# Optimization experiments

Measured on AMD Instinct MI355X. Metric: run time of the kernel, lower is better.

## Reference

```python
import jax, jax.numpy as jnp
import numpy as np
import math

B, S, SIG, EMB, LAT, H, L_ENC, L_DEC = 16, 1024, 256, 256, 256, 8, 2, 2
EH, DH = EMB // H, LAT // H
EPS = 1e-10


def _sinusoidal_last_row(d):
    # last row of a standard sinusoidal PE table (position index = max_len-1)
    pos = 5000.0 - 1.0
    i = np.arange(d)
    angles = pos / np.power(10000.0, (2 * (i // 2)) / d)
    pe = np.where(i % 2 == 0, np.sin(angles), np.cos(angles))
    return jnp.asarray(pe, dtype=jnp.float32)


def setup_inputs() -> dict:
    key = jax.random.key(0)
    ks = iter(jax.random.split(key, 64))
    w = lambda *sh: 0.05 * jax.random.normal(next(ks), sh, dtype=jnp.float32)
    z = lambda *sh: jnp.zeros(sh, dtype=jnp.float32)
    d = {
        'inputData': jax.random.normal(next(ks), (B, S, SIG), dtype=jnp.float32),
        'pos_enc': _sinusoidal_last_row(SIG),
        'embW': w(SIG, EMB), 'embb': z(EMB),
        'qW': w(EMB, EMB), 'qb': z(EMB),
        'kW': w(EMB, EMB), 'kb': z(EMB),
        'vW': w(EMB, EMB), 'vb': z(EMB),
        'encBW': w(EH, EH), 'encBb': z(EH),
        'oW': w(EMB, EMB), 'ob': z(EMB),
        'ffe_W1': w(EMB, 2 * EMB), 'ffe_b1': z(2 * EMB),
        'ffe_W2': w(2 * EMB, EMB), 'ffe_b2': z(EMB),
        'lnSA_g': jnp.ones((L_ENC, EMB)), 'lnSA_b': z(L_ENC, EMB),
        'lnFF_g': jnp.ones((L_ENC, EMB)), 'lnFF_b': z(L_ENC, EMB),
        'start': w(1, LAT),
        'decQW': w(LAT, LAT), 'decQb': z(LAT),
        'decKW': w(EMB, EMB), 'decKb': z(EMB),
        'decVW': w(EMB, LAT), 'decVb': z(LAT),
        'decBW': w(EH + DH, DH), 'decBb': z(DH),
        'latW': w(LAT, LAT), 'latb': z(LAT),
        'ffd_W1': w(LAT, LAT // 2), 'ffd_b1': z(LAT // 2),
        'ffd_W2': w(LAT // 2, LAT), 'ffd_b2': z(LAT),
        'lnCA_g': jnp.ones((L_DEC, LAT)), 'lnCA_b': z(L_DEC, LAT),
        'lnLFF_g': jnp.ones((L_DEC, LAT)), 'lnLFF_b': z(L_DEC, LAT),
        'finW': w(LAT, LAT), 'finb': z(LAT),
    }
    return d


def _ln(x, g, b):
    m = x.mean(-1, keepdims=True)
    v = x.var(-1, keepdims=True)
    return (x - m) * jax.lax.rsqrt(v + EPS) * g + b


def _enc_attn(x, qW, qb, kW, kb, vW, vb, bW, bb, oW, ob):
    # x: (B,S,EMB) -> heads (B,H,S,EH)
    sp = lambda t: t.reshape(B, S, H, EH).transpose(0, 2, 1, 3)
    q, k, v = sp(x @ qW + qb), sp(x @ kW + kb), sp(x @ vW + vb)
    bk = k @ bW + bb                                   # bilinear key (B,H,S,EH)
    attn = jax.nn.softmax(jnp.einsum('bhqd,bhkd->bhqk', q, bk) / math.sqrt(EH), axis=-1)
    out = jnp.einsum('bhqk,bhkd->bhqd', attn, v)
    out = out.transpose(0, 2, 1, 3).reshape(B, S, EMB)
    return out @ oW + ob


def _dec_attn(enc, lat, qW, qb, kW, kb, vW, vb, bW, bb, oW, ob):
    # lat: (B,LAT) single query token; enc: (B,S,EMB)
    q = (lat @ qW + qb).reshape(B, 1, H, DH).transpose(0, 2, 1, 3)   # (B,H,1,DH)
    k = (enc @ kW + kb).reshape(B, S, H, EH).transpose(0, 2, 1, 3)   # (B,H,S,EH)
    v = (enc @ vW + vb).reshape(B, S, H, DH).transpose(0, 2, 1, 3)   # (B,H,S,DH)
    qcat = jnp.broadcast_to(q, (B, H, S, DH))
    kcat = jnp.concatenate([k, qcat], axis=-1)                       # (B,H,S,EH+DH)
    bk = kcat @ bW + bb                                              # (B,H,S,DH)
    attn = jax.nn.softmax(jnp.einsum('bhqd,bhkd->bhqk', q, bk) / math.sqrt(EH + DH), axis=-1)
    out = jnp.einsum('bhqk,bhkd->bhqd', attn, v)                     # (B,H,1,DH)
    out = out.transpose(0, 2, 1, 3).reshape(B, LAT)
    return out @ oW + ob


def reference(inputData, pos_enc, embW, embb, qW, qb, kW, kb, vW, vb, encBW, encBb,
              oW, ob, ffe_W1, ffe_b1, ffe_W2, ffe_b2, lnSA_g, lnSA_b, lnFF_g, lnFF_b,
              start, decQW, decQb, decKW, decKb, decVW, decVb, decBW, decBb,
              latW, latb, ffd_W1, ffd_b1, ffd_W2, ffd_b2, lnCA_g, lnCA_b,
              lnLFF_g, lnLFF_b, finW, finb):
    emb = (inputData + pos_enc) @ embW + embb          # (B,S,EMB)
    t = emb
    for l in range(L_ENC):
        n = _ln(t, lnSA_g[l], lnSA_b[l])
        a = _enc_attn(n, qW, qb, kW, kb, vW, vb, encBW, encBb, oW, ob) + n
        t = a + emb
        n2 = _ln(t, lnFF_g[l], lnFF_b[l])
        ff = jax.nn.selu(n2 @ ffe_W1 + ffe_b1) @ ffe_W2 + ffe_b2
        t = ff + n2
    init_lat = jnp.broadcast_to(start, (B, LAT))
    lat = init_lat
    for l in range(L_DEC):
        nl = _ln(init_lat, lnCA_g[l], lnCA_b[l])       # module always feeds initialLatentData
        lat = _dec_attn(t, nl, decQW, decQb, decKW, decKb, decVW, decVb,
                        decBW, decBb, latW, latb)
        nf = _ln(lat, lnLFF_g[l], lnLFF_b[l])
        lat = jax.nn.selu(nf @ ffd_W1 + ffd_b1) @ ffd_W2 + ffd_b2
    return lat @ finW + finb
```

## Files before the change

### kernel.cpp

```cpp
#include <hip/hip_runtime.h>
#include <hip/hip_bf16.h>
#include <math.h>

typedef __hip_bfloat16 bf16;

#define BB 16
#define SS 1024
#define NH 8
#define NR (BB*SS)
#define SZE ((size_t)NR*256)
#define RS 264
#define HS 520

typedef __attribute__((ext_vector_type(8))) short short8;
typedef __attribute__((ext_vector_type(4))) float f32x4;
typedef __attribute__((ext_vector_type(8))) unsigned short u16x8;
typedef __attribute__((ext_vector_type(4))) unsigned short u16x4;

__device__ __forceinline__ float bf2f(bf16 x){ return __bfloat162float(x); }
__device__ __forceinline__ bf16  f2bf(float x){ return __float2bfloat16(x); }
__device__ __forceinline__ unsigned short f2bfu(float x){
  bf16 t = __float2bfloat16(x); return *reinterpret_cast<unsigned short*>(&t);
}
__device__ __forceinline__ float bfu2f(unsigned short u){
  return __uint_as_float(((unsigned)u)<<16);
}

__device__ __forceinline__ float ldT(const float* p, size_t i){ return p[i]; }
__device__ __forceinline__ float ldT(const bf16*  p, size_t i){ return bf2f(p[i]); }
__device__ __forceinline__ void  stT(float* p, size_t i, float v){ p[i] = v; }
__device__ __forceinline__ void  stT(bf16*  p, size_t i, float v){ p[i] = f2bf(v); }

__device__ __forceinline__ float selu_f(float x){
  const float a = 1.6732632423543772f, sc = 1.0507009873554805f;
  return sc * (x > 0.f ? x : a * expm1f(x));
}

__device__ __forceinline__ void gload16(const void* g, void* l){
  __builtin_amdgcn_global_load_lds(
      (const __attribute__((address_space(1))) unsigned int*)g,
      (__attribute__((address_space(3))) unsigned int*)l, 16, 0, 0);
}

struct PtrPack { const void* p[43]; };
struct TabPack { int off[43]; int cnt[43]; int total; };
struct TrTab   { int srcOff[12]; int K[12]; int N[12]; int dstOff[12]; int total; };

__global__ __launch_bounds__(256) void k_canon(PtrPack ptrs, TabPack tab,
    float* __restrict__ dst, int* __restrict__ flagw)
{
  unsigned w0 = ((const unsigned*)ptrs.p[18])[0];
  int isbf = (w0 == 0x3F803F80u) ? 1 : 0;
  if (blockIdx.x == 0 && threadIdx.x == 0) *flagw = isbf;
  __shared__ int so[43], sn[43];
  int tid = threadIdx.x;
  if (tid < 43){ so[tid] = tab.off[tid]; sn[tid] = tab.cnt[tid]; }
  __syncthreads();
  int g = blockIdx.x*256 + tid;
  if (g >= tab.total) return;
  int seg = 1;
  while (seg < 42 && g >= so[seg] + sn[seg]) seg++;
  int li = g - so[seg];
  float v = isbf ? bf2f(((const bf16*)ptrs.p[seg])[li])
                 : ((const float*)ptrs.p[seg])[li];
  dst[g] = v;
}

__global__ __launch_bounds__(256) void k_transW(const float* __restrict__ wt,
    TrTab tt, unsigned short* __restrict__ dst)
{
  int g = blockIdx.x*256 + threadIdx.x;
  if (g >= tt.total) return;
  int seg = 0;
  while (seg < 11 && g >= tt.dstOff[seg] + tt.K[seg]*tt.N[seg]) seg++;
  int li = g - tt.dstOff[seg];
  int K = tt.K[seg], N = tt.N[seg];
  int n = li / K, k = li - n*K;
  dst[g] = f2bfu(wt[tt.srcOff[seg] + (size_t)k*N + n]);
}

__global__ __launch_bounds__(256) void k_qfold(const float* __restrict__ wt,
    int qOff, int qbOff, int bwOff, unsigned short* __restrict__ qW2t,
    float* __restrict__ qbf)
{
  __shared__ float bw[32];
  int n = blockIdx.x, t = threadIdx.x;
  int h = n>>5, d = n&31;
  if (t < 32) bw[t] = wt[bwOff + d*32 + t];
  __syncthreads();
  float acc = 0.f;
  #pragma unroll 8
  for (int j = 0; j < 32; j++) acc += wt[qOff + (size_t)t*256 + h*32 + j]*bw[j];
  qW2t[(size_t)n*256 + t] = f2bfu(acc);
  if (t == 0){
    float a = 0.f;
    #pragma unroll 8
    for (int j = 0; j < 32; j++) a += wt[qbOff + h*32 + j]*bw[j];
    qbf[n] = a;
  }
}

template<int K, int LDA, int CT>
__device__ __forceinline__ void wave_gemmN(const unsigned short (*As)[LDA],
    const unsigned short* __restrict__ Wt, int n0, f32x4 acc[4][CT], int lane)
{
  int col = lane & 15, quad = lane >> 4;
  #pragma unroll
  for (int k0 = 0; k0 < K; k0 += 32){
    short8 a[4], b[CT];
    #pragma unroll
    for (int rt = 0; rt < 4; rt++)
      a[rt] = *(const short8*)(&As[rt*16 + col][k0 + quad*8]);
    #pragma unroll
    for (int ct = 0; ct < CT; ct++)
      b[ct] = *(const short8*)(&Wt[(size_t)(n0 + ct*16 + col)*K + k0 + quad*8]);
    #pragma unroll
    for (int rt = 0; rt < 4; rt++)
      #pragma unroll
      for (int ct = 0; ct < CT; ct++)
        acc[rt][ct] = __builtin_amdgcn_mfma_f32_16x16x32_bf16(a[rt], b[ct], acc[rt][ct], 0, 0, 0);
  }
}

template<int K, int LDA, int CT>
__device__ __forceinline__ void wave_gemmM32(const unsigned short (*As)[LDA],
    const unsigned short* __restrict__ Wt, int n0, f32x4 acc[2][CT], int lane)
{
  int col = lane & 15, quad = lane >> 4;
  #pragma unroll
  for (int k0 = 0; k0 < K; k0 += 32){
    short8 a[2], b[CT];
    #pragma unroll
    for (int rt = 0; rt < 2; rt++)
      a[rt] = *(const short8*)(&As[rt*16 + col][k0 + quad*8]);
    #pragma unroll
    for (int ct = 0; ct < CT; ct++)
      b[ct] = *(const short8*)(&Wt[(size_t)(n0 + ct*16 + col)*K + k0 + quad*8]);
    #pragma unroll
    for (int rt = 0; rt < 2; rt++)
      #pragma unroll
      for (int ct = 0; ct < CT; ct++)
        acc[rt][ct] = __builtin_amdgcn_mfma_f32_16x16x32_bf16(a[rt], b[ct], acc[rt][ct], 0, 0, 0);
  }
}

#define ZERO_ACC4(acc)  { _Pragma("unroll") for (int rt=0;rt<4;rt++){ _Pragma("unroll") for (int ct=0;ct<4;ct++) acc[rt][ct] = (f32x4){0.f,0.f,0.f,0.f}; } }
#define ZERO_ACC2(acc)  { _Pragma("unroll") for (int rt=0;rt<4;rt++){ _Pragma("unroll") for (int ct=0;ct<2;ct++) acc[rt][ct] = (f32x4){0.f,0.f,0.f,0.f}; } }
#define ZERO_ACC24(acc) { _Pragma("unroll") for (int rt=0;rt<2;rt++){ _Pragma("unroll") for (int ct=0;ct<4;ct++) acc[rt][ct] = (f32x4){0.f,0.f,0.f,0.f}; } }

#define EPI_BEGIN(e) { int rt = (e)>>4, ct = ((e)>>2)&3, r = (e)&3; \
    int lrow = rt*16 + quad*4 + r; int gcol0 = ct*16 + col; \
    float av = acc[rt][ct][r]; (void)lrow; (void)gcol0; (void)av;
#define EPI_END }

#define EPI32_BEGIN(e) { int rt = (e)>>4, ct = ((e)>>2)&3, r = (e)&3; \
    int lrow = rt*16 + quad*4 + r; int gcol0 = ct*16 + col; \
    float av = acc[rt][ct][r]; (void)lrow; (void)gcol0; (void)av;
#define EPI32_END }

template<int PRE, typename OT>
__global__ __launch_bounds__(256) void k_gemm_mfma(const void* __restrict__ A,
    const int* __restrict__ flagp, const float* __restrict__ pe,
    const unsigned short* __restrict__ Wt, const float* __restrict__ bias,
    OT* __restrict__ out)
{
  __shared__ __align__(16) unsigned short As[64][RS];
  int tid = threadIdx.x;
  int m = blockIdx.x & 255, nh = blockIdx.x >> 8;
  int row0 = m*64;
  if (PRE == 0){
    int f = *flagp;
    for (int jj = 0; jj < 64; jj++){
      int idx = tid + jj*256, row = idx>>8, c = idx&255;
      size_t g = (size_t)(row0+row)*256 + c;
      float x = f ? bf2f(((const bf16*)A)[g]) : ((const float*)A)[g];
      As[row][c] = f2bfu(x + pe[c]);
    }
  } else {
    for (int jj = 0; jj < 16; jj++){
      int idx = tid + jj*256;
      int row = idx>>6, c4 = (idx&63)<<2;
      float4 x = *(const float4*)((const float*)A + (size_t)(row0+row)*256 + c4);
      *(u16x4*)(&As[row][c4]) = (u16x4){f2bfu(x.x),f2bfu(x.y),f2bfu(x.z),f2bfu(x.w)};
    }
  }
  __syncthreads();
  int w = tid>>6, lane = tid&63, col = lane&15, quad = lane>>4;
  int n0 = nh*128 + w*32;
  f32x4 acc[4][2];
  ZERO_ACC2(acc);
  wave_gemmN<256, RS, 2>(As, Wt, n0, acc, lane);
  #pragma unroll
  for (int rt = 0; rt < 4; rt++){
    #pragma unroll
    for (int ct = 0; ct < 2; ct++){
      #pragma unroll
      for (int r = 0; r < 4; r++){
        int grow = row0 + rt*16 + quad*4 + r;
        int gcol = n0 + ct*16 + col;
        stT(out, (size_t)grow*256 + gcol, acc[rt][ct][r] + bias[gcol]);
      }
    }
  }
}

__global__ __launch_bounds__(256) void k_decKV(const float* __restrict__ A,
    const unsigned short* __restrict__ KWt, const float* __restrict__ kb,
    const unsigned short* __restrict__ VWt, const float* __restrict__ vb,
    bf16* __restrict__ ko, bf16* __restrict__ vo)
{
  __shared__ __align__(16) unsigned short As[64][RS];
  int tid = threadIdx.x;
  int m = blockIdx.x & 255, nh = blockIdx.x >> 8;
  int row0 = m*64;
  for (int jj = 0; jj < 16; jj++){
    int idx = tid + jj*256;
    int row = idx>>6, c4 = (idx&63)<<2;
    float4 x = *(const float4*)(A + (size_t)(row0+row)*256 + c4);
    *(u16x4*)(&As[row][c4]) = (u16x4){f2bfu(x.x),f2bfu(x.y),f2bfu(x.z),f2bfu(x.w)};
  }
  __syncthreads();
  int w = tid>>6, lane = tid&63, col = lane&15, quad = lane>>4;
  int n0 = nh*128 + w*32;
  f32x4 acc[4][2];
  ZERO_ACC2(acc);
  wave_gemmN<256, RS, 2>(As, KWt, n0, acc, lane);
  #pragma unroll
  for (int rt = 0; rt < 4; rt++){
    #pragma unroll
    for (int ct = 0; ct < 2; ct++){
      #pragma unroll
      for (int r = 0; r < 4; r++){
        int grow = row0 + rt*16 + quad*4 + r;
        int gcol = n0 + ct*16 + col;
        ko[(size_t)grow*256 + gcol] = f2bf(acc[rt][ct][r] + kb[gcol]);
      }
    }
  }
  ZERO_ACC2(acc);
  wave_gemmN<256, RS, 2>(As, VWt, n0, acc, lane);
  #pragma unroll
  for (int rt = 0; rt < 4; rt++){
    #pragma unroll
    for (int ct = 0; ct < 2; ct++){
      #pragma unroll
      for (int r = 0; r < 4; r++){
        int grow = row0 + rt*16 + quad*4 + r;
        int gcol = n0 + ct*16 + col;
        vo[(size_t)grow*256 + gcol] = f2bf(acc[rt][ct][r] + vb[gcol]);
      }
    }
  }
}

__global__ __launch_bounds__(256) void k_qkvbk_mfma(const float* __restrict__ tsrc,
    const float* __restrict__ lng, const float* __restrict__ lnb,
    const unsigned short* __restrict__ qW2t, const float* __restrict__ qbf,
    const unsigned short* __restrict__ kWt, const float* __restrict__ kb,
    const unsigned short* __restrict__ vWt, const float* __restrict__ vb,
    bf16* __restrict__ qo, bf16* __restrict__ vo, bf16* __restrict__ bko)
{
  __shared__ __align__(16) unsigned short Ns[64][RS];
  __shared__ float mArr[64], rArr[64];
  int tid = threadIdx.x;
  int m = blockIdx.x & 255, nh = blockIdx.x >> 8;
  int row0 = m*64;
  int b = row0 >> 10, s0 = row0 & 1023;
  {
    int row = tid>>2, l4 = tid&3;
    const float4* rp = (const float4*)(tsrc + (size_t)(row0+row)*256) + l4*16;
    float s = 0.f, s2 = 0.f;
    #pragma unroll 4
    for (int c = 0; c < 16; c++){
      float4 x = rp[c];
      s += x.x + x.y + x.z + x.w;
      s2 += x.x*x.x + x.y*x.y + x.z*x.z + x.w*x.w;
    }
    s  += __shfl_down(s, 2, 4);  s  += __shfl_down(s, 1, 4);
    s2 += __shfl_down(s2, 2, 4); s2 += __shfl_down(s2, 1, 4);
    if (l4 == 0){
      float mn = s*(1.f/256.f);
      float v = s2*(1.f/256.f) - mn*mn;
      mArr[row] = mn; rArr[row] = rsqrtf(fmaxf(v,0.f) + 1e-10f);
    }
  }
  __syncthreads();
  for (int jj = 0; jj < 16; jj++){
    int idx = tid + jj*256;
    int row = idx>>6, c4 = (idx&63)<<2;
    float4 x = *(const float4*)(tsrc + (size_t)(row0+row)*256 + c4);
    float mn = mArr[row], rr = rArr[row];
    u16x4 o;
    o[0] = f2bfu((x.x - mn)*rr*lng[c4+0] + lnb[c4+0]);
    o[1] = f2bfu((x.y - mn)*rr*lng[c4+1] + lnb[c4+1]);
    o[2] = f2bfu((x.z - mn)*rr*lng[c4+2] + lnb[c4+2]);
    o[3] = f2bfu((x.w - mn)*rr*lng[c4+3] + lnb[c4+3]);
    *(u16x4*)(&Ns[row][c4]) = o;
  }
  __syncthreads();
  int w = tid>>6, lane = tid&63, col = lane&15, quad = lane>>4;
  int n0 = nh*128 + w*32;
  f32x4 acc[4][2];
  ZERO_ACC2(acc);
  wave_gemmN<256, RS, 2>(Ns, qW2t, n0, acc, lane);
  #pragma unroll
  for (int rt = 0; rt < 4; rt++){
    #pragma unroll
    for (int ct = 0; ct < 2; ct++){
      #pragma unroll
      for (int r = 0; r < 4; r++){
        int grow = row0 + rt*16 + quad*4 + r;
        int gcol = n0 + ct*16 + col;
        qo[(size_t)grow*256 + gcol] = f2bf(acc[rt][ct][r] + qbf[gcol]);
      }
    }
  }
  ZERO_ACC2(acc);
  wave_gemmN<256, RS, 2>(Ns, vWt, n0, acc, lane);
  #pragma unroll
  for (int rt = 0; rt < 4; rt++){
    #pragma unroll
    for (int ct = 0; ct < 2; ct++){
      #pragma unroll
      for (int r = 0; r < 4; r++){
        int grow = row0 + rt*16 + quad*4 + r;
        int gcol = n0 + ct*16 + col;
        vo[(size_t)grow*256 + gcol] = f2bf(acc[rt][ct][r] + vb[gcol]);
      }
    }
  }
  ZERO_ACC2(acc);
  wave_gemmN<256, RS, 2>(Ns, kWt, n0, acc, lane);
  int h = nh*4 + w;
  #pragma unroll
  for (int rt = 0; rt < 4; rt++){
    #pragma unroll
    for (int ct = 0; ct < 2; ct++){
      #pragma unroll
      for (int r = 0; r < 4; r++){
        int srow = s0 + rt*16 + quad*4 + r;
        int d = ct*16 + col;
        bko[(((size_t)(b*NH+h))*SS + srow)*32 + d] =
            f2bf(acc[rt][ct][r] + kb[h*32 + d]);
      }
    }
  }
}

__global__ __launch_bounds__(256) void k_attn_mfma(
    const bf16* __restrict__ q, const bf16* __restrict__ bk,
    const bf16* __restrict__ v, bf16* __restrict__ ao)
{
  int bi = blockIdx.x;
  int qq = bi >> 7, b = (bi >> 3) & 15, h = bi & 7;
  int tid = threadIdx.x;
  int w = tid>>6, lane = tid&63;
  int quad = lane>>4, col = lane&15;
  int q0 = qq*128 + w*32;

  __shared__ __align__(16) unsigned short Ks2b[2][64][32];
  __shared__ __align__(16) unsigned short Vt2b[2][32][76];

  const float scale2 = 0.17677669529663687f * 1.4426950408889634f;
  short8 aq[2];
  #pragma unroll
  for (int rt = 0; rt < 2; rt++){
    const unsigned short* gq = (const unsigned short*)q
        + ((size_t)(b*SS + q0 + rt*16 + col))*256 + h*32 + quad*8;
    u16x8 qv = *(const u16x8*)gq;
    #pragma unroll
    for (int i=0;i<8;i++) aq[rt][i] = (short)f2bfu(bfu2f(qv[i])*scale2);
  }

  float l_r[2] = {0.f, 0.f};
  f32x4 o[2][2];
  #pragma unroll
  for (int rt=0;rt<2;rt++)
    #pragma unroll
    for (int ct=0;ct<2;ct++) o[rt][ct] = (f32x4){0.f,0.f,0.f,0.f};

  int krow = tid>>2, ksl = tid&3;
  int kslw = ksl ^ ((krow>>1)&3);
  int vk0 = tid>>3, vdg = tid&7;
  int vk1 = vk0 + 32;
  int rsl = (quad ^ ((col>>1)&3))*8;

  const unsigned short* bkp = (const unsigned short*)bk + ((size_t)(b*NH+h))*SS*32;
  const unsigned short* vp  = (const unsigned short*)v + (size_t)b*SS*256 + h*32;

  u16x8 rK;
  u16x4 rV0, rV1;
  rK  = *(const u16x8*)(bkp + (size_t)krow*32 + ksl*8);
  rV0 = *(const u16x4*)(vp + (size_t)vk0*256 + vdg*4);
  rV1 = *(const u16x4*)(vp + (size_t)vk1*256 + vdg*4);

  for (int kt = 0; kt < 16; kt++){
    int cb = kt & 1;
    *(u16x8*)(&Ks2b[cb][krow][kslw*8]) = rK;
    #pragma unroll
    for (int i=0;i<4;i++) Vt2b[cb][vdg*4+i][vk0] = rV0[i];
    #pragma unroll
    for (int i=0;i<4;i++) Vt2b[cb][vdg*4+i][vk1] = rV1[i];
    __syncthreads();
    if (kt < 15){
      int nk = kt + 1;
      rK  = *(const u16x8*)(bkp + (size_t)(nk*64 + krow)*32 + ksl*8);
      rV0 = *(const u16x4*)(vp + (size_t)(nk*64 + vk0)*256 + vdg*4);
      rV1 = *(const u16x4*)(vp + (size_t)(nk*64 + vk1)*256 + vdg*4);
    }
    #pragma unroll
    for (int g = 0; g < 2; g++){
      unsigned pk[2][4];
      #pragma unroll
      for (int tt = 0; tt < 2; tt++){
        int t4 = g*2 + tt;
        short8 bk8 = *(const short8*)(&Ks2b[cb][t4*16 + col][rsl]);
        #pragma unroll
        for (int rt = 0; rt < 2; rt++){
          f32x4 s = __builtin_amdgcn_mfma_f32_16x16x32_bf16(bk8, aq[rt],
                      (f32x4){0.f,0.f,0.f,0.f}, 0, 0, 0);
          float e0 = __builtin_amdgcn_exp2f(s[0]);
          float e1 = __builtin_amdgcn_exp2f(s[1]);
          float e2 = __builtin_amdgcn_exp2f(s[2]);
          float e3 = __builtin_amdgcn_exp2f(s[3]);
          l_r[rt] += (e0+e1)+(e2+e3);
          pk[rt][tt*2+0] = __builtin_amdgcn_perm(
              __float_as_uint(e1), __float_as_uint(e0), 0x07060302u);
          pk[rt][tt*2+1] = __builtin_amdgcn_perm(
// ... 25 lines not shown
  for (int rt=0;rt<2;rt++){
    float l = l_r[rt];
    l += __shfl_xor(l, 16, 64);
    l += __shfl_xor(l, 32, 64);
    float inv = 1.f / l;
    size_t obase = ((size_t)(b*SS + q0 + rt*16 + col))*256 + h*32;
    #pragma unroll
    for (int ct=0;ct<2;ct++){
      u16x4 ov;
      #pragma unroll
      for (int r=0;r<4;r++) ov[r] = f2bfu(o[rt][ct][r]*inv);
      *(u16x4*)((unsigned short*)ao + obase + ct*16 + quad*4) = ov;
    }
  }
}

__global__ __launch_bounds__(256) void k_oln_mfma(
    const float* __restrict__ tsrc, const float* __restrict__ emb,
    const bf16* __restrict__ ao,
    const float* __restrict__ lnSAg, const float* __restrict__ lnSAb,
    const unsigned short* __restrict__ oWt, const float* __restrict__ ob,
    const float* __restrict__ lnFFg, const float* __restrict__ lnFFb,
    bf16* __restrict__ n2o)
{
  __shared__ __align__(16) unsigned short Aos[32][RS];
  __shared__ __align__(16) unsigned short Tm[32][RS];
  __shared__ float mArr[32], rArr[32];
  int tid = threadIdx.x, row0 = blockIdx.x*32;
  {
    int row = tid>>3, l8 = tid&7;
    const float* rp = tsrc + (size_t)(row0+row)*256;
    float s = 0.f, s2 = 0.f;
    for (int c = l8; c < 256; c += 8){ float x = rp[c]; s += x; s2 += x*x; }
    s  += __shfl_down(s, 4, 8);  s  += __shfl_down(s, 2, 8);  s  += __shfl_down(s, 1, 8);
    s2 += __shfl_down(s2, 4, 8); s2 += __shfl_down(s2, 2, 8); s2 += __shfl_down(s2, 1, 8);
    if (l8 == 0){
      float m = s*(1.f/256.f);
      float v = s2*(1.f/256.f) - m*m;
      mArr[row] = m; rArr[row] = rsqrtf(fmaxf(v,0.f) + 1e-10f);
    }
  }
  for (int jj = 0; jj < 4; jj++){
    int idx = tid + jj*256;
    int row = idx>>5, c8 = idx&31;
    *(u16x8*)(&Aos[row][c8*8]) =
        *(const u16x8*)((const unsigned short*)ao + (size_t)(row0+row)*256 + c8*8);
  }
  __syncthreads();
  int w = tid>>6, lane = tid&63, col = lane&15, quad = lane>>4;
  f32x4 acc[2][4];
  ZERO_ACC24(acc);
  wave_gemmM32<256, RS, 4>(Aos, oWt, w*64, acc, lane);
  #pragma unroll
  for (int e = 0; e < 32; e++){
    EPI32_BEGIN(e)
    int gcol = w*64 + gcol0;
    size_t g = (size_t)(row0+lrow)*256 + gcol;
    float n1 = (tsrc[g] - mArr[lrow])*rArr[lrow]*lnSAg[gcol] + lnSAb[gcol];
    Tm[lrow][gcol] = f2bfu(av + ob[gcol] + n1 + emb[g]);
    EPI32_END
  }
  __syncthreads();
  {
    int row = tid>>3, l8 = tid&7;
    float s = 0.f, s2 = 0.f;
    for (int c = l8; c < 256; c += 8){ float x = bfu2f(Tm[row][c]); s += x; s2 += x*x; }
    s  += __shfl_down(s, 4, 8);  s  += __shfl_down(s, 2, 8);  s  += __shfl_down(s, 1, 8);
    s2 += __shfl_down(s2, 4, 8); s2 += __shfl_down(s2, 2, 8); s2 += __shfl_down(s2, 1, 8);
    if (l8 == 0){
      float m = s*(1.f/256.f);
      float v = s2*(1.f/256.f) - m*m;
      mArr[row] = m; rArr[row] = rsqrtf(fmaxf(v,0.f) + 1e-10f);
    }
  }
  __syncthreads();
  for (int jj = 0; jj < 32; jj++){
    int idx = tid + jj*256, row = idx>>8, c = idx&255;
    float x = bfu2f(Tm[row][c]);
    n2o[(size_t)(row0+row)*256 + c] =
        f2bf((x - mArr[row])*rArr[row]*lnFFg[c] + lnFFb[c]);
  }
}

#define FF_STAGE(B, KT) { \
  int k0 = (KT)*64; \
  _Pragma("unroll") \
  for (int i = 0; i < 4; i++){ int c = w*4 + i; \
    gload16(A  + (size_t)(row0 + c*8 + rsub)*KFULL + k0 + sgo, &As[B][c*512]); } \
  _Pragma("unroll") \
  for (int i = 0; i < 2; i++){ int c = w*2 + i; \
    gload16(Wb + (size_t)(n0   + c*8 + rsub)*KFULL + k0 + sgo, &Bs[B][c*512]); } }

#define FF_COMPUTE(B) { \
  _Pragma("unroll") \
  for (int kk = 0; kk < 2; kk++){ \
    short8 a[4], b2r[2]; \
    _Pragma("unroll") \
    for (int rt = 0; rt < 4; rt++) \
      a[rt] = *(const short8*)(&As[B][((wr*64 + rt*16 + col)<<6) + ((((kk<<2)|quad) ^ (col&7))<<3)]); \
    _Pragma("unroll") \
    for (int ct = 0; ct < 2; ct++) \
      b2r[ct] = *(const short8*)(&Bs[B][((wc*32 + ct*16 + col)<<6) + ((((kk<<2)|quad) ^ (col&7))<<3)]); \
    _Pragma("unroll") \
    for (int rt = 0; rt < 4; rt++) \
      _Pragma("unroll") \
      for (int ct = 0; ct < 2; ct++) \
        acc[rt][ct] = __builtin_amdgcn_mfma_f32_16x16x32_bf16(a[rt], b2r[ct], acc[rt][ct], 0, 0, 0); } }

template<int KFULL, int NFULL, int EPI>
__global__ __launch_bounds__(256) void k_ff_gemm(const bf16* __restrict__ A,
    const unsigned short* __restrict__ Wt, const float* __restrict__ bias,
    const bf16* __restrict__ res, void* __restrict__ outv)
{
  __shared__ __align__(16) unsigned short As[2][128*64];
  __shared__ __align__(16) unsigned short Bs[2][64*64];
  constexpr int NWG = 128 * (NFULL/64);
  constexpr int NKT = KFULL/64;
  int tid = threadIdx.x;
  int w = tid>>6, lane = tid&63;
  int col = lane&15, quad = lane>>4;
  int wr = w>>1, wc = w&1;
  int rsub = lane>>3;
  int sgo = (((lane&7) ^ rsub)<<3);
  int bid = blockIdx.x;
  int swz = (bid & 7)*(NWG>>3) + (bid >> 3);
  int mb = swz & 127, nb = swz >> 7;
  int row0 = mb*128, n0 = nb*64;
  const bf16* Wb = (const bf16*)Wt;

  f32x4 acc[4][2];
  ZERO_ACC2(acc);

  FF_STAGE(0, 0);
  __syncthreads();
  #pragma unroll
  for (int kt = 0; kt < NKT-1; kt++){
    int cb = kt & 1;
    FF_STAGE(cb^1, kt+1);
    FF_COMPUTE(cb);
    __syncthreads();
  }
  FF_COMPUTE((NKT-1)&1);

  if (EPI == 0){
    bf16* o = (bf16*)outv;
    #pragma unroll
    for (int rt = 0; rt < 4; rt++){
      #pragma unroll
      for (int ct = 0; ct < 2; ct++){
        #pragma unroll
        for (int r = 0; r < 4; r++){
          int grow = row0 + wr*64 + rt*16 + quad*4 + r;
          int gcol = n0 + wc*32 + ct*16 + col;
          o[(size_t)grow*NFULL + gcol] = f2bf(selu_f(acc[rt][ct][r] + bias[gcol]));
        }
      }
    }
  } else {
    float* o = (float*)outv;
    #pragma unroll
    for (int rt = 0; rt < 4; rt++){
      #pragma unroll
      for (int ct = 0; ct < 2; ct++){
        #pragma unroll
        for (int r = 0; r < 4; r++){
          int grow = row0 + wr*64 + rt*16 + quad*4 + r;
          int gcol = n0 + wc*32 + ct*16 + col;
          size_t g = (size_t)grow*NFULL + gcol;
          o[g] = acc[rt][ct][r] + bias[gcol] + bf2f(res[g]);
        }
      }
    }
  }
}

__global__ __launch_bounds__(256) void k_dec_head(const float* __restrict__ startp,
    const float* __restrict__ lng, const float* __restrict__ lnb,
    const float* __restrict__ decQW, const float* __restrict__ decQb,
    const float* __restrict__ decBW,
    float* __restrict__ s_q, float* __restrict__ s_qc)
{
  __shared__ float s1[256], s2[256], nl[256], qv[256];
  int t = threadIdx.x;
  float v = startp[t];
  s1[t]=v; s2[t]=v*v; __syncthreads();
  for (int s=128;s>0;s>>=1){
    if (t<s){ s1[t]+=s1[t+s]; s2[t]+=s2[t+s]; }
    __syncthreads();
  }
  float m = s1[0]*(1.f/256.f);
  float var = s2[0]*(1.f/256.f) - m*m;
  float r = rsqrtf(fmaxf(var,0.f) + 1e-10f);
  nl[t] = (v-m)*r*lng[t] + lnb[t];
  __syncthreads();
  float acc = decQb[t];
  for (int k=0;k<256;k++) acc += nl[k]*decQW[k*256+t];
  qv[t] = acc; s_q[t] = acc;
  __syncthreads();
  int h = t>>5, d = t&31;
  float a = 0.f;
  #pragma unroll 8
  for (int e=0;e<32;e++) a += qv[h*32+e]*decBW[(32+e)*32 + d];
  s_qc[t] = a;
}

__global__ __launch_bounds__(256) void k_bkdec_mfma(const bf16* __restrict__ kk,
    const float* __restrict__ qc, const unsigned short* __restrict__ decBWt,
    const float* __restrict__ Bb, bf16* __restrict__ bko)
{
  __shared__ __align__(16) unsigned short Ks[64][RS];
  int tid = threadIdx.x, row0 = blockIdx.x*64;
  int b = row0 >> 10, s0 = row0 & 1023;
  for (int jj = 0; jj < 8; jj++){
    int idx = tid + jj*256;
    int row = idx>>5, c8 = idx&31;
    *(u16x8*)(&Ks[row][c8*8]) =
        *(const u16x8*)((const unsigned short*)kk + (size_t)(row0+row)*256 + c8*8);
  }
  __syncthreads();
  int w = tid>>6, lane = tid&63, col = lane&15, quad = lane>>4;
  f32x4 acc[4][4];
  ZERO_ACC4(acc);
  #pragma unroll
  for (int ct = 0; ct < 4; ct++){
    int base = w*64 + ct*16;
    int h = base >> 5, d0 = base & 31;
    short8 bfrag = *(const short8*)(&decBWt[(size_t)(d0 + col)*32 + quad*8]);
    #pragma unroll
    for (int rt = 0; rt < 4; rt++){
      short8 afrag = *(const short8*)(&Ks[rt*16 + col][h*32 + quad*8]);
      acc[rt][ct] = __builtin_amdgcn_mfma_f32_16x16x32_bf16(afrag, bfrag, acc[rt][ct], 0, 0, 0);
    }
  }
  #pragma unroll
  for (int e = 0; e < 64; e++){
    EPI_BEGIN(e)
    int srow = s0 + lrow;
    int gcol = w*64 + gcol0;
    int h = gcol >> 5, d = gcol & 31;
    bko[(((size_t)(b*NH+h))*SS + srow)*32 + d] = f2bf(av + qc[gcol] + Bb[d]);
    EPI_END
  }
}

__global__ __launch_bounds__(256) void k_attn_dec(const float* __restrict__ q,
    const bf16* __restrict__ bk, const bf16* __restrict__ v,
    float* __restrict__ out)
{
  int h = blockIdx.x & 7, b = blockIdx.x >> 3;
  int tid = threadIdx.x;
  __shared__ float qs[32];
  __shared__ float sc[SS];
  __shared__ float red[256];
  if (tid < 32) qs[tid] = q[h*32 + tid] * (0.125f * 1.4426950408889634f);
  __syncthreads();
  float lsum = 0.f;
  for (int jj=0;jj<4;jj++){
    int j = tid*4 + jj;
// ... 14 lines not shown
    acc += sc[j]*bf2f(v[((size_t)(b*SS + j))*256 + h*32 + d]);
  red[c*32+d] = acc;
  __syncthreads();
  if (tid < 32){
    float s = 0.f;
    #pragma unroll
    for (int cc=0;cc<8;cc++) s += red[cc*32+tid];
    out[b*256 + h*32 + tid] = s / gs;
  }
}

__global__ __launch_bounds__(256) void k_dec_tail(const float* __restrict__ s_ao,
    const float* __restrict__ latW, const float* __restrict__ latb,
    const float* __restrict__ lng, const float* __restrict__ lnb,
    const float* __restrict__ W1, const float* __restrict__ b1,
    const float* __restrict__ W2, const float* __restrict__ b2,
    const float* __restrict__ finW, const float* __restrict__ finb,
    const int* __restrict__ flagp, void* __restrict__ outv)
{
  __shared__ float x[256], y[256], s1[256], s2[256];
  int t = threadIdx.x, b = blockIdx.x;
  x[t] = s_ao[b*256 + t];
  __syncthreads();
  float lat = latb[t];
  for (int k=0;k<256;k++) lat += x[k]*latW[k*256+t];
  s1[t]=lat; s2[t]=lat*lat; __syncthreads();
  for (int s=128;s>0;s>>=1){
    if (t<s){ s1[t]+=s1[t+s]; s2[t]+=s2[t+s]; }
    __syncthreads();
  }
  float m = s1[0]*(1.f/256.f);
  float var = s2[0]*(1.f/256.f) - m*m;
  float r = rsqrtf(fmaxf(var,0.f) + 1e-10f);
  y[t] = (lat-m)*r*lng[t] + lnb[t];
  __syncthreads();
  if (t < 128){
    float a2 = b1[t];
    for (int k=0;k<256;k++) a2 += y[k]*W1[k*128+t];
    x[t] = selu_f(a2);
  }
  __syncthreads();
  float a3 = b2[t];
  for (int k=0;k<128;k++) a3 += x[k]*W2[k*256+t];
  s1[t] = a3;
  __syncthreads();
  float o = finb[t];
  for (int k=0;k<256;k++) o += s1[k]*finW[k*256+t];
  size_t oi = (size_t)b*256 + t;
  if (*flagp) ((bf16*)outv)[oi] = f2bf(o);
  else        ((float*)outv)[oi] = o;
}

extern "C" void kernel_launch(void* const* d_in, const int* in_sizes, int n_in,
                              void* d_out, int out_size, void* d_ws, size_t ws_size,
                              hipStream_t stream)
{
  static const int cnts[43] = {
    0,256,65536,256,65536,256,65536,256,65536,256,1024,32,65536,256,
    131072,512,131072,256,512,512,512,512,256,65536,256,65536,256,65536,256,
    2048,32,65536,256,32768,128,32768,256,512,512,512,512,65536,256 };
  TabPack tab; int acc0 = 0;
  for (int i = 0; i < 43; i++){ tab.off[i] = acc0; tab.cnt[i] = cnts[i]; acc0 += cnts[i]; }
  tab.total = acc0;
  PtrPack ptrs;
  for (int i = 0; i < 43; i++) ptrs.p[i] = d_in[i];

  char* p = (char*)d_ws;
  float* wt   = (float*)p;
  int*  flagp = (int*)(p + (4u<<20));
  char* bigc  = p + (4u<<20) + 256;
  float* g_emb = (float*)bigc;
  float* g_t   = (float*)(bigc + SZE*4);
  bf16*  g_q   = (bf16*)(bigc + 2*SZE*4);
  bf16*  g_v   = (bf16*)(bigc + 2*SZE*4 + SZE*2);
  bf16*  g_ao  = (bf16*)(bigc + 2*SZE*4 + 2*SZE*2);
  bf16*  g_bk  = (bf16*)(bigc + 2*SZE*4 + 3*SZE*2);
  float* fsm   = (float*)(bigc + 2*SZE*4 + 4*SZE*2);
  unsigned short* wtr = (unsigned short*)(bigc + 2*SZE*4 + 4*SZE*2 + 131072*4);
  float* s_q  = fsm;
  float* s_qc = fsm + 256;
  float* s_ao = fsm + 512;
  float* qbf  = fsm + 8192;
  bf16*  g_h1 = g_v;

  static const int trIdx[10] = {2,4,6,8,12,14,16,25,27,10};
  static const int trK[10]   = {256,256,256,256,256,256,512,256,256,32};
  static const int trN[10]   = {256,256,256,256,256,512,256,256,256,32};
  TrTab tr; int tacc = 0;
  for (int i = 0; i < 10; i++){
    tr.srcOff[i] = tab.off[trIdx[i]];
    tr.K[i] = trK[i]; tr.N[i] = trN[i];
    tr.dstOff[i] = tacc; tacc += trK[i]*trN[i];
  }
  tr.srcOff[10] = tab.off[29];        tr.K[10]=32; tr.N[10]=32; tr.dstOff[10]=tacc; tacc+=1024;
  tr.srcOff[11] = tab.off[29] + 1024; tr.K[11]=32; tr.N[11]=32; tr.dstOff[11]=tacc; tacc+=1024;
  tr.total = tacc;
  const unsigned short *embWt = wtr + tr.dstOff[0],
    *kWt = wtr + tr.dstOff[2], *vWt = wtr + tr.dstOff[3], *oWt = wtr + tr.dstOff[4],
    *ffeW1t = wtr + tr.dstOff[5], *ffeW2t = wtr + tr.dstOff[6],
    *decKWt = wtr + tr.dstOff[7], *decVWt = wtr + tr.dstOff[8],
    *decBWtk = wtr + tr.dstOff[10];
  unsigned short* qW2t = wtr + tr.total;

  #define WP(i) (wt + tab.off[i])
  const float *pe=WP(1), *embb=WP(3), *qb=WP(5), *kb=WP(7), *vb=WP(9),
    *ob=WP(13), *ffeb1=WP(15), *ffeb2=WP(17),
    *lnSAg=WP(18), *lnSAb=WP(19), *lnFFg=WP(20), *lnFFb=WP(21),
    *startp=WP(22), *decQW=WP(23), *decQb=WP(24), *decKb=WP(26),
    *decVb=WP(28), *decBW=WP(29), *decBb=WP(30), *latW=WP(31),
    *latb=WP(32), *ffdW1=WP(33), *ffdb1=WP(34), *ffdW2=WP(35), *ffdb2=WP(36),
    *lnCAg=WP(37), *lnCAb=WP(38), *lnLFFg=WP(39), *lnLFFb=WP(40),
    *finW=WP(41), *finb=WP(42);

  dim3 blk(256);
  const int G64  = NR/64;
  const int G32  = NR/32;
  const int GSP  = 512;
  const int GA2  = 1024;
  const int LD   = 1;

  k_canon<<<(tab.total+255)/256, blk, 0, stream>>>(ptrs, tab, wt, flagp);
  k_transW<<<(tr.total+255)/256, blk, 0, stream>>>(wt, tr, wtr);
  k_qfold<<<256, blk, 0, stream>>>(wt, tab.off[4], tab.off[5], tab.off[10], qW2t, qbf);

  k_gemm_mfma<0,float><<<GSP, blk, 0, stream>>>(d_in[0], flagp, pe, embWt, embb, g_emb);

  const float* tcur = g_emb;
  for (int l = 0; l < 2; l++){
    k_qkvbk_mfma<<<GSP, blk, 0, stream>>>(tcur, lnSAg+l*256, lnSAb+l*256,
        qW2t, qbf, kWt, kb, vWt, vb, g_q, g_v, g_bk);
    k_attn_mfma<<<GA2, blk, 0, stream>>>(g_q, g_bk, g_v, g_ao);
    k_oln_mfma<<<G32, blk, 0, stream>>>(tcur, g_emb, g_ao,
        lnSAg+l*256, lnSAb+l*256, oWt, ob, lnFFg+l*256, lnFFb+l*256, g_q);
    k_ff_gemm<256,512,0><<<1024, blk, 0, stream>>>(g_q, ffeW1t, ffeb1, (const bf16*)nullptr, g_h1);
    k_ff_gemm<512,256,1><<<512, blk, 0, stream>>>(g_h1, ffeW2t, ffeb2, g_q, g_t);
    tcur = g_t;
  }

  k_dec_head<<<1, blk, 0, stream>>>(startp, lnCAg+LD*256, lnCAb+LD*256,
      decQW, decQb, decBW, s_q, s_qc);
  k_decKV<<<GSP, blk, 0, stream>>>(g_t, decKWt, decKb, decVWt, decVb, g_q, g_v);
  k_bkdec_mfma<<<G64, blk, 0, stream>>>(g_q, s_qc, decBWtk, decBb, g_bk);
  k_attn_dec<<<BB*NH, blk, 0, stream>>>(s_q, g_bk, g_v, s_ao);
  k_dec_tail<<<BB, blk, 0, stream>>>(s_ao, latW, latb, lnLFFg+LD*256, lnLFFb+LD*256,
      ffdW1, ffdb1, ffdW2, ffdb2, finW, finb, flagp, d_out);
  #undef WP
}
```

Measured before the change: 501.0 us.

## Split LN from QKV projection and reuse pipelined FF GEMM for QKV and decoder KV

The fused LayerNorm+QKV kernel is split into a standalone LayerNorm kernel that writes bf16, followed by a concatenated QKV GEMM built on the double-buffered global_load_lds FF GEMM machinery with 128x64 tiles. The decoder K/V projection likewise moves to this pipelined GEMM. It now reads a bf16 copy of the final encoder output, which the last FF2 epilogue writes. The aim is to replace the older kernels, which staged all of K=256 in LDS with no pipelining, with the faster tiled GEMM path. The cost is an extra bf16 round trip through global memory for the normalized activations and an extra bf16 store in the last FF2 kernel. The weight-transpose table is reorganized so K, V and folded Q weights sit contiguously, and the transpose kernel's segment search bound is lowered to match.

```diff
diff --git a/kernel.cpp b/kernel.cpp
--- a/kernel.cpp
+++ b/kernel.cpp
@@ -10,7 +10,6 @@
 #define NR (BB*SS)
 #define SZE ((size_t)NR*256)
 #define RS 264
-#define HS 520
 
 typedef __attribute__((ext_vector_type(8))) short short8;
 typedef __attribute__((ext_vector_type(4))) float f32x4;
@@ -26,10 +25,8 @@
   return __uint_as_float(((unsigned)u)<<16);
 }
 
-__device__ __forceinline__ float ldT(const float* p, size_t i){ return p[i]; }
-__device__ __forceinline__ float ldT(const bf16*  p, size_t i){ return bf2f(p[i]); }
-__device__ __forceinline__ void  stT(float* p, size_t i, float v){ p[i] = v; }
-__device__ __forceinline__ void  stT(bf16*  p, size_t i, float v){ p[i] = f2bf(v); }
+__device__ __forceinline__ void stT(float* p, size_t i, float v){ p[i] = v; }
+__device__ __forceinline__ void stT(bf16*  p, size_t i, float v){ p[i] = f2bf(v); }
 
 __device__ __forceinline__ float selu_f(float x){
   const float a = 1.6732632423543772f, sc = 1.0507009873554805f;
@@ -72,7 +69,7 @@
   int g = blockIdx.x*256 + threadIdx.x;
   if (g >= tt.total) return;
   int seg = 0;
-  while (seg < 11 && g >= tt.dstOff[seg] + tt.K[seg]*tt.N[seg]) seg++;
+  while (seg < 8 && g >= tt.dstOff[seg] + tt.K[seg]*tt.N[seg]) seg++;
   int li = g - tt.dstOff[seg];
   int K = tt.K[seg], N = tt.N[seg];
   int n = li / K, k = li - n*K;
@@ -204,68 +201,12 @@
   }
 }
 
-__global__ __launch_bounds__(256) void k_decKV(const float* __restrict__ A,
-    const unsigned short* __restrict__ KWt, const float* __restrict__ kb,
-    const unsigned short* __restrict__ VWt, const float* __restrict__ vb,
-    bf16* __restrict__ ko, bf16* __restrict__ vo)
-{
-  __shared__ __align__(16) unsigned short As[64][RS];
-  int tid = threadIdx.x;
-  int m = blockIdx.x & 255, nh = blockIdx.x >> 8;
-  int row0 = m*64;
-  for (int jj = 0; jj < 16; jj++){
-    int idx = tid + jj*256;
-    int row = idx>>6, c4 = (idx&63)<<2;
-    float4 x = *(const float4*)(A + (size_t)(row0+row)*256 + c4);
-    *(u16x4*)(&As[row][c4]) = (u16x4){f2bfu(x.x),f2bfu(x.y),f2bfu(x.z),f2bfu(x.w)};
-  }
-  __syncthreads();
-  int w = tid>>6, lane = tid&63, col = lane&15, quad = lane>>4;
-  int n0 = nh*128 + w*32;
-  f32x4 acc[4][2];
-  ZERO_ACC2(acc);
-  wave_gemmN<256, RS, 2>(As, KWt, n0, acc, lane);
-  #pragma unroll
-  for (int rt = 0; rt < 4; rt++){
-    #pragma unroll
-    for (int ct = 0; ct < 2; ct++){
-      #pragma unroll
-      for (int r = 0; r < 4; r++){
-        int grow = row0 + rt*16 + quad*4 + r;
-        int gcol = n0 + ct*16 + col;
-        ko[(size_t)grow*256 + gcol] = f2bf(acc[rt][ct][r] + kb[gcol]);
-      }
-    }
-  }
-  ZERO_ACC2(acc);
-  wave_gemmN<256, RS, 2>(As, VWt, n0, acc, lane);
-  #pragma unroll
-  for (int rt = 0; rt < 4; rt++){
-    #pragma unroll
-    for (int ct = 0; ct < 2; ct++){
-      #pragma unroll
-      for (int r = 0; r < 4; r++){
-        int grow = row0 + rt*16 + quad*4 + r;
-        int gcol = n0 + ct*16 + col;
-        vo[(size_t)grow*256 + gcol] = f2bf(acc[rt][ct][r] + vb[gcol]);
-      }
-    }
-  }
-}
-
-__global__ __launch_bounds__(256) void k_qkvbk_mfma(const float* __restrict__ tsrc,
+__global__ __launch_bounds__(256) void k_ln(const float* __restrict__ tsrc,
     const float* __restrict__ lng, const float* __restrict__ lnb,
-    const unsigned short* __restrict__ qW2t, const float* __restrict__ qbf,
-    const unsigned short* __restrict__ kWt, const float* __restrict__ kb,
-    const unsigned short* __restrict__ vWt, const float* __restrict__ vb,
-    bf16* __restrict__ qo, bf16* __restrict__ vo, bf16* __restrict__ bko)
-{
-  __shared__ __align__(16) unsigned short Ns[64][RS];
+    bf16* __restrict__ out)
+{
   __shared__ float mArr[64], rArr[64];
-  int tid = threadIdx.x;
-  int m = blockIdx.x & 255, nh = blockIdx.x >> 8;
-  int row0 = m*64;
-  int b = row0 >> 10, s0 = row0 & 1023;
+  int tid = threadIdx.x, row0 = blockIdx.x*64;
   {
     int row = tid>>2, l4 = tid&3;
     const float4* rp = (const float4*)(tsrc + (size_t)(row0+row)*256) + l4*16;
@@ -295,55 +236,161 @@
     o[1] = f2bfu((x.y - mn)*rr*lng[c4+1] + lnb[c4+1]);
     o[2] = f2bfu((x.z - mn)*rr*lng[c4+2] + lnb[c4+2]);
     o[3] = f2bfu((x.w - mn)*rr*lng[c4+3] + lnb[c4+3]);
-    *(u16x4*)(&Ns[row][c4]) = o;
-  }
-  __syncthreads();
-  int w = tid>>6, lane = tid&63, col = lane&15, quad = lane>>4;
-  int n0 = nh*128 + w*32;
-  f32x4 acc[4][2];
-  ZERO_ACC2(acc);
-  wave_gemmN<256, RS, 2>(Ns, qW2t, n0, acc, lane);
-  #pragma unroll
-  for (int rt = 0; rt < 4; rt++){
-    #pragma unroll
-    for (int ct = 0; ct < 2; ct++){
-      #pragma unroll
-      for (int r = 0; r < 4; r++){
-        int grow = row0 + rt*16 + quad*4 + r;
-        int gcol = n0 + ct*16 + col;
-        qo[(size_t)grow*256 + gcol] = f2bf(acc[rt][ct][r] + qbf[gcol]);
-      }
-    }
-  }
-  ZERO_ACC2(acc);
-  wave_gemmN<256, RS, 2>(Ns, vWt, n0, acc, lane);
-  #pragma unroll
-  for (int rt = 0; rt < 4; rt++){
-    #pragma unroll
-    for (int ct = 0; ct < 2; ct++){
-      #pragma unroll
-      for (int r = 0; r < 4; r++){
-        int grow = row0 + rt*16 + quad*4 + r;
-        int gcol = n0 + ct*16 + col;
-        vo[(size_t)grow*256 + gcol] = f2bf(acc[rt][ct][r] + vb[gcol]);
-      }
-    }
-  }
-  ZERO_ACC2(acc);
-  wave_gemmN<256, RS, 2>(Ns, kWt, n0, acc, lane);
-  int h = nh*4 + w;
-  #pragma unroll
-  for (int rt = 0; rt < 4; rt++){
-    #pragma unroll
-    for (int ct = 0; ct < 2; ct++){
-      #pragma unroll
-      for (int r = 0; r < 4; r++){
-        int srow = s0 + rt*16 + quad*4 + r;
-        int d = ct*16 + col;
-        bko[(((size_t)(b*NH+h))*SS + srow)*32 + d] =
-            f2bf(acc[rt][ct][r] + kb[h*32 + d]);
-      }
-    }
+    *(u16x4*)((unsigned short*)out + (size_t)(row0+row)*256 + c4) = o;
+  }
+}
+
+#define FF_STAGE(B, KT) { \
+  int k0 = (KT)*64; \
+  _Pragma("unroll") \
+  for (int i = 0; i < 4; i++){ int c = w*4 + i; \
+    gload16(A  + (size_t)(row0 + c*8 + rsub)*KFULL + k0 + sgo, &As[B][c*512]); } \
+  _Pragma("unroll") \
+  for (int i = 0; i < 2; i++){ int c = w*2 + i; \
+    gload16(Wb + (size_t)(n0   + c*8 + rsub)*KFULL + k0 + sgo, &Bs[B][c*512]); } }
+
+#define FF_COMPUTE(B) { \
+  _Pragma("unroll") \
+  for (int kk = 0; kk < 2; kk++){ \
+    short8 a[4], b2r[2]; \
+    _Pragma("unroll") \
+    for (int rt = 0; rt < 4; rt++) \
+      a[rt] = *(const short8*)(&As[B][((wr*64 + rt*16 + col)<<6) + ((((kk<<2)|quad) ^ (col&7))<<3)]); \
+    _Pragma("unroll") \
+    for (int ct = 0; ct < 2; ct++) \
+      b2r[ct] = *(const short8*)(&Bs[B][((wc*32 + ct*16 + col)<<6) + ((((kk<<2)|quad) ^ (col&7))<<3)]); \
+    _Pragma("unroll") \
+    for (int rt = 0; rt < 4; rt++) \
+      _Pragma("unroll") \
+      for (int ct = 0; ct < 2; ct++) \
+        acc[rt][ct] = __builtin_amdgcn_mfma_f32_16x16x32_bf16(a[rt], b2r[ct], acc[rt][ct], 0, 0, 0); } }
+
+#define FF_PROLOG() \
+  __shared__ __align__(16) unsigned short As[2][128*64]; \
+  __shared__ __align__(16) unsigned short Bs[2][64*64]; \
+  int tid = threadIdx.x; \
+  int w = tid>>6, lane = tid&63; \
+  int col = lane&15, quad = lane>>4; \
+  int wr = w>>1, wc = w&1; \
+  int rsub = lane>>3; \
+  int sgo = (((lane&7) ^ rsub)<<3); \
+  int bid = blockIdx.x; \
+  int swz = (bid & 7)*(NWG>>3) + (bid >> 3); \
+  int mb = swz & 127, nb = swz >> 7; \
+  int row0 = mb*128, n0 = nb*64; \
+  f32x4 acc[4][2]; \
+  ZERO_ACC2(acc); \
+  FF_STAGE(0, 0); \
+  __syncthreads(); \
+  _Pragma("unroll") \
+  for (int kt = 0; kt < NKT-1; kt++){ \
+    int cb = kt & 1; \
+    FF_STAGE(cb^1, kt+1); \
+    FF_COMPUTE(cb); \
+    __syncthreads(); \
+  } \
+  FF_COMPUTE((NKT-1)&1);
+
+#define FF_EPI_LOOP(body) \
+  _Pragma("unroll") \
+  for (int rt = 0; rt < 4; rt++){ \
+    _Pragma("unroll") \
+    for (int ct = 0; ct < 2; ct++){ \
+      _Pragma("unroll") \
+      for (int r = 0; r < 4; r++){ \
+        int grow = row0 + wr*64 + rt*16 + quad*4 + r; \
+        int lcol = wc*32 + ct*16 + col; \
+        float av = acc[rt][ct][r]; \
+        body \
+      } } }
+
+template<int KFULL, int NFULL, int EPI>
+__global__ __launch_bounds__(256) void k_ff_gemm(const bf16* __restrict__ A,
+    const unsigned short* __restrict__ Wt, const float* __restrict__ bias,
+    const bf16* __restrict__ res, void* __restrict__ outv, bf16* __restrict__ outb)
+{
+  constexpr int NWG = 128 * (NFULL/64);
+  constexpr int NKT = KFULL/64;
+  const bf16* Wb = (const bf16*)Wt;
+  FF_PROLOG()
+  if (EPI == 0){
+    bf16* o = (bf16*)outv;
+    FF_EPI_LOOP({
+      int gcol = n0 + lcol;
+      o[(size_t)grow*NFULL + gcol] = f2bf(selu_f(av + bias[gcol]));
+    })
+  } else if (EPI == 1){
+    float* o = (float*)outv;
+    FF_EPI_LOOP({
+      int gcol = n0 + lcol;
+      size_t g = (size_t)grow*NFULL + gcol;
+      o[g] = av + bias[gcol] + bf2f(res[g]);
+    })
+  } else {
+    float* o = (float*)outv;
+    FF_EPI_LOOP({
+      int gcol = n0 + lcol;
+      size_t g = (size_t)grow*NFULL + gcol;
+      float val = av + bias[gcol] + bf2f(res[g]);
+      o[g] = val;
+      outb[g] = f2bf(val);
+    })
+  }
+}
+
+__global__ __launch_bounds__(256) void k_qkv_gemm(const bf16* __restrict__ A,
+    const unsigned short* __restrict__ Wt,
+    const float* __restrict__ vb, const float* __restrict__ kb,
+    const float* __restrict__ qbf,
+    bf16* __restrict__ qo, bf16* __restrict__ vo, bf16* __restrict__ bko)
+{
+  constexpr int KFULL = 256;
+  constexpr int NWG = 128 * 12;
+  constexpr int NKT = 4;
+  const bf16* Wb = (const bf16*)Wt;
+  FF_PROLOG()
+  if (n0 < 256){
+    FF_EPI_LOOP({
+      int gcol = n0 + lcol;
+      vo[(size_t)grow*256 + gcol] = f2bf(av + vb[gcol]);
+    })
+  } else if (n0 < 512){
+    FF_EPI_LOOP({
+      int kcol = n0 - 256 + lcol;
+      int h = kcol>>5;
+      int d = kcol&31;
+      int b = grow>>10;
+      int srow = grow&1023;
+      bko[(((size_t)(b*NH+h))*SS + srow)*32 + d] = f2bf(av + kb[kcol]);
+    })
+  } else {
+    FF_EPI_LOOP({
+      int qcol = n0 - 512 + lcol;
+      qo[(size_t)grow*256 + qcol] = f2bf(av + qbf[qcol]);
+    })
+  }
+}
+
+__global__ __launch_bounds__(256) void k_decKV_gemm(const bf16* __restrict__ A,
+    const unsigned short* __restrict__ Wt,
+    const float* __restrict__ kbd, const float* __restrict__ vbd,
+    bf16* __restrict__ ko, bf16* __restrict__ vo)
+{
+  constexpr int KFULL = 256;
+  constexpr int NWG = 128 * 8;
+  constexpr int NKT = 4;
+  const bf16* Wb = (const bf16*)Wt;
+  FF_PROLOG()
+  if (n0 < 256){
+    FF_EPI_LOOP({
+      int gcol = n0 + lcol;
+      ko[(size_t)grow*256 + gcol] = f2bf(av + kbd[gcol]);
+    })
+  } else {
+    FF_EPI_LOOP({
+      int gcol = n0 - 256 + lcol;
+      vo[(size_t)grow*256 + gcol] = f2bf(av + vbd[gcol]);
+    })
   }
 }
 
@@ -535,98 +582,6 @@
   }
 }
 
-#define FF_STAGE(B, KT) { \
-  int k0 = (KT)*64; \
-  _Pragma("unroll") \
-  for (int i = 0; i < 4; i++){ int c = w*4 + i; \
-    gload16(A  + (size_t)(row0 + c*8 + rsub)*KFULL + k0 + sgo, &As[B][c*512]); } \
-  _Pragma("unroll") \
-  for (int i = 0; i < 2; i++){ int c = w*2 + i; \
-    gload16(Wb + (size_t)(n0   + c*8 + rsub)*KFULL + k0 + sgo, &Bs[B][c*512]); } }
-
-#define FF_COMPUTE(B) { \
-  _Pragma("unroll") \
-  for (int kk = 0; kk < 2; kk++){ \
-    short8 a[4], b2r[2]; \
-    _Pragma("unroll") \
-    for (int rt = 0; rt < 4; rt++) \
-      a[rt] = *(const short8*)(&As[B][((wr*64 + rt*16 + col)<<6) + ((((kk<<2)|quad) ^ (col&7))<<3)]); \
-    _Pragma("unroll") \
-    for (int ct = 0; ct < 2; ct++) \
-      b2r[ct] = *(const short8*)(&Bs[B][((wc*32 + ct*16 + col)<<6) + ((((kk<<2)|quad) ^ (col&7))<<3)]); \
-    _Pragma("unroll") \
-    for (int rt = 0; rt < 4; rt++) \
-      _Pragma("unroll") \
-      for (int ct = 0; ct < 2; ct++) \
-        acc[rt][ct] = __builtin_amdgcn_mfma_f32_16x16x32_bf16(a[rt], b2r[ct], acc[rt][ct], 0, 0, 0); } }
-
-template<int KFULL, int NFULL, int EPI>
-__global__ __launch_bounds__(256) void k_ff_gemm(const bf16* __restrict__ A,
-    const unsigned short* __restrict__ Wt, const float* __restrict__ bias,
-    const bf16* __restrict__ res, void* __restrict__ outv)
-{
-  __shared__ __align__(16) unsigned short As[2][128*64];
-  __shared__ __align__(16) unsigned short Bs[2][64*64];
-  constexpr int NWG = 128 * (NFULL/64);
-  constexpr int NKT = KFULL/64;
-  int tid = threadIdx.x;
-  int w = tid>>6, lane = tid&63;
-  int col = lane&15, quad = lane>>4;
-  int wr = w>>1, wc = w&1;
-  int rsub = lane>>3;
-  int sgo = (((lane&7) ^ rsub)<<3);
-  int bid = blockIdx.x;
-  int swz = (bid & 7)*(NWG>>3) + (bid >> 3);
-  int mb = swz & 127, nb = swz >> 7;
-  int row0 = mb*128, n0 = nb*64;
-  const bf16* Wb = (const bf16*)Wt;
-
-  f32x4 acc[4][2];
-  ZERO_ACC2(acc);
-
-  FF_STAGE(0, 0);
-  __syncthreads();
-  #pragma unroll
-  for (int kt = 0; kt < NKT-1; kt++){
-    int cb = kt & 1;
-    FF_STAGE(cb^1, kt+1);
-    FF_COMPUTE(cb);
-    __syncthreads();
-  }
-  FF_COMPUTE((NKT-1)&1);
-
-  if (EPI == 0){
-    bf16* o = (bf16*)outv;
-    #pragma unroll
-    for (int rt = 0; rt < 4; rt++){
-      #pragma unroll
-      for (int ct = 0; ct < 2; ct++){
-        #pragma unroll
-        for (int r = 0; r < 4; r++){
-          int grow = row0 + wr*64 + rt*16 + quad*4 + r;
-          int gcol = n0 + wc*32 + ct*16 + col;
-          o[(size_t)grow*NFULL + gcol] = f2bf(selu_f(acc[rt][ct][r] + bias[gcol]));
-        }
-      }
-    }
-  } else {
-    float* o = (float*)outv;
-    #pragma unroll
-    for (int rt = 0; rt < 4; rt++){
-      #pragma unroll
-      for (int ct = 0; ct < 2; ct++){
-        #pragma unroll
-        for (int r = 0; r < 4; r++){
-          int grow = row0 + wr*64 + rt*16 + quad*4 + r;
-          int gcol = n0 + wc*32 + ct*16 + col;
-          size_t g = (size_t)grow*NFULL + gcol;
-          o[g] = acc[rt][ct][r] + bias[gcol] + bf2f(res[g]);
-        }
-      }
-    }
-  }
-}
-
 __global__ __launch_bounds__(256) void k_dec_head(const float* __restrict__ startp,
     const float* __restrict__ lng, const float* __restrict__ lnb,
     const float* __restrict__ decQW, const float* __restrict__ decQb,
@@ -807,28 +762,31 @@
   float* s_ao = fsm + 512;
   float* qbf  = fsm + 8192;
   bf16*  g_h1 = g_v;
-
-  static const int trIdx[10] = {2,4,6,8,12,14,16,25,27,10};
-  static const int trK[10]   = {256,256,256,256,256,256,512,256,256,32};
-  static const int trN[10]   = {256,256,256,256,256,512,256,256,256,32};
+  bf16*  g_n  = g_ao;
+  bf16*  g_tb = g_bk;
+
+  static const int trIdx[6] = {2,12,14,16,25,27};
+  static const int trK[6]   = {256,256,256,512,256,256};
+  static const int trN[6]   = {256,256,512,256,256,256};
   TrTab tr; int tacc = 0;
-  for (int i = 0; i < 10; i++){
+  for (int i = 0; i < 6; i++){
     tr.srcOff[i] = tab.off[trIdx[i]];
     tr.K[i] = trK[i]; tr.N[i] = trN[i];
     tr.dstOff[i] = tacc; tacc += trK[i]*trN[i];
   }
-  tr.srcOff[10] = tab.off[29];        tr.K[10]=32; tr.N[10]=32; tr.dstOff[10]=tacc; tacc+=1024;
-  tr.srcOff[11] = tab.off[29] + 1024; tr.K[11]=32; tr.N[11]=32; tr.dstOff[11]=tacc; tacc+=1024;
+  tr.srcOff[6] = tab.off[29]; tr.K[6]=32;  tr.N[6]=32;  tr.dstOff[6]=tacc; tacc+=1024;
+  tr.srcOff[7] = tab.off[8];  tr.K[7]=256; tr.N[7]=256; tr.dstOff[7]=tacc; tacc+=65536;
+  tr.srcOff[8] = tab.off[6];  tr.K[8]=256; tr.N[8]=256; tr.dstOff[8]=tacc; tacc+=65536;
   tr.total = tacc;
-  const unsigned short *embWt = wtr + tr.dstOff[0],
-    *kWt = wtr + tr.dstOff[2], *vWt = wtr + tr.dstOff[3], *oWt = wtr + tr.dstOff[4],
-    *ffeW1t = wtr + tr.dstOff[5], *ffeW2t = wtr + tr.dstOff[6],
-    *decKWt = wtr + tr.dstOff[7], *decVWt = wtr + tr.dstOff[8],
-    *decBWtk = wtr + tr.dstOff[10];
-  unsigned short* qW2t = wtr + tr.total;
+  const unsigned short *embWt = wtr + tr.dstOff[0], *oWt = wtr + tr.dstOff[1],
+    *ffeW1t = wtr + tr.dstOff[2], *ffeW2t = wtr + tr.dstOff[3],
+    *wdec = wtr + tr.dstOff[4],
+    *decBWtk = wtr + tr.dstOff[6],
+    *wqkv = wtr + tr.dstOff[7];
+  unsigned short* qW2t = (unsigned short*)wqkv + 512*256;
 
   #define WP(i) (wt + tab.off[i])
-  const float *pe=WP(1), *embb=WP(3), *qb=WP(5), *kb=WP(7), *vb=WP(9),
+  const float *pe=WP(1), *embb=WP(3), *kb=WP(7), *vb=WP(9),
     *ob=WP(13), *ffeb1=WP(15), *ffeb2=WP(17),
     *lnSAg=WP(18), *lnSAb=WP(19), *lnFFg=WP(20), *lnFFb=WP(21),
     *startp=WP(22), *decQW=WP(23), *decQb=WP(24), *decKb=WP(26),
@@ -852,19 +810,25 @@
 
   const float* tcur = g_emb;
   for (int l = 0; l < 2; l++){
-    k_qkvbk_mfma<<<GSP, blk, 0, stream>>>(tcur, lnSAg+l*256, lnSAb+l*256,
-        qW2t, qbf, kWt, kb, vWt, vb, g_q, g_v, g_bk);
+    k_ln<<<G64, blk, 0, stream>>>(tcur, lnSAg+l*256, lnSAb+l*256, g_n);
+    k_qkv_gemm<<<1536, blk, 0, stream>>>(g_n, wqkv, vb, kb, qbf, g_q, g_v, g_bk);
     k_attn_mfma<<<GA2, blk, 0, stream>>>(g_q, g_bk, g_v, g_ao);
     k_oln_mfma<<<G32, blk, 0, stream>>>(tcur, g_emb, g_ao,
         lnSAg+l*256, lnSAb+l*256, oWt, ob, lnFFg+l*256, lnFFb+l*256, g_q);
-    k_ff_gemm<256,512,0><<<1024, blk, 0, stream>>>(g_q, ffeW1t, ffeb1, (const bf16*)nullptr, g_h1);
-    k_ff_gemm<512,256,1><<<512, blk, 0, stream>>>(g_h1, ffeW2t, ffeb2, g_q, g_t);
+    k_ff_gemm<256,512,0><<<1024, blk, 0, stream>>>(g_q, ffeW1t, ffeb1,
+        (const bf16*)nullptr, g_h1, (bf16*)nullptr);
+    if (l == 0)
+      k_ff_gemm<512,256,1><<<512, blk, 0, stream>>>(g_h1, ffeW2t, ffeb2,
+          g_q, g_t, (bf16*)nullptr);
+    else
+      k_ff_gemm<512,256,2><<<512, blk, 0, stream>>>(g_h1, ffeW2t, ffeb2,
+          g_q, g_t, g_tb);
     tcur = g_t;
   }
 
   k_dec_head<<<1, blk, 0, stream>>>(startp, lnCAg+LD*256, lnCAb+LD*256,
       decQW, decQb, decBW, s_q, s_qc);
-  k_decKV<<<GSP, blk, 0, stream>>>(g_t, decKWt, decKb, decVWt, decVb, g_q, g_v);
+  k_decKV_gemm<<<1024, blk, 0, stream>>>(g_tb, wdec, decKb, decVb, g_q, g_v);
   k_bkdec_mfma<<<G64, blk, 0, stream>>>(g_q, s_qc, decBWtk, decBb, g_bk);
   k_attn_dec<<<BB*NH, blk, 0, stream>>>(s_q, g_bk, g_v, s_ao);
   k_dec_tail<<<BB, blk, 0, stream>>>(s_ao, latW, latb, lnLFFg+LD*256, lnLFFb+LD*256,
```

Measured after the change: 519.4 us. +3.7%, slower.
